# Kernel optimization log

Hardware: AMD Instinct MI355X
Metric: run time of the kernel (lower is better)

The kernel has to match this reference:

```python
import jax, jax.numpy as jnp
import numpy as np

NUM_HEADS = 16

def setup_inputs() -> dict:
    key = jax.random.key(0)
    ks = jax.random.split(key, 6)
    B, S, D = 4, 1024, 1024
    scale = 1.0 / np.sqrt(D)
    return {
        "query": jax.random.normal(ks[0], (B, S, D), jnp.float32),
        "key":   jax.random.normal(ks[1], (B, S, D), jnp.float32),
        "value": jax.random.normal(ks[2], (B, S, D), jnp.float32),
        "Wq": jax.random.normal(ks[3], (D, D), jnp.float32) * scale,
        "bq": jnp.zeros((D,), jnp.float32),
        "Wk": jax.random.normal(ks[4], (D, D), jnp.float32) * scale,
        "bk": jnp.zeros((D,), jnp.float32),
        "Wv": jax.random.normal(ks[5], (D, D), jnp.float32) * scale,
        "bv": jnp.zeros((D,), jnp.float32),
    }

def reference(query, key, value, Wq, bq, Wk, bk, Wv, bv):
    B, Sq, D = query.shape
    Sk = key.shape[1]
    H = NUM_HEADS
    dh = D // H
    # QKV projections -> (B, S, H, dh)
    q = (query @ Wq + bq).reshape(B, Sq, H, dh)
    k = (key   @ Wk + bk).reshape(B, Sk, H, dh)
    v = (value @ Wv + bv).reshape(B, Sk, H, dh)
    inv_sqrt = 1.0 / jnp.sqrt(jnp.asarray(dh, q.dtype))
    # scores: (B, H, Sq, Sk) -- attention matrix explicitly materialized (as in source)
    scores = jnp.einsum('bqhd,bkhd->bhqk', q, k) * inv_sqrt
    attn = jax.nn.softmax(scores, axis=-1)
    # context: (B, Sq, H, dh) -> (B, Sq, D)
    context = jnp.einsum('bhqk,bkhd->bqhd', attn, v).reshape(B, Sq, D)
    # source returns attn in heads-major (num_heads*batch, Sq, Sk) layout
    attn_out = jnp.transpose(attn, (1, 0, 2, 3)).reshape(H * B, Sq, Sk)
    return context, attn_out
```

## Files before the change

### kernel.cpp

```cpp
#include <hip/hip_runtime.h>

#define BB 4
#define SS 1024
#define DD 1024
#define HH 16
#define DHH 64
#define MT (BB*SS)

typedef __bf16 bf16x8 __attribute__((ext_vector_type(8)));
typedef unsigned short u16x8 __attribute__((ext_vector_type(8)));
typedef unsigned short u16x4 __attribute__((ext_vector_type(4)));
typedef float f32x4 __attribute__((ext_vector_type(4)));

__device__ __forceinline__ bf16x8 as_bf16x8(u16x8 u) {
  union { u16x8 u; bf16x8 b; } c; c.u = u; return c.b;
}
__device__ __forceinline__ unsigned short f2bf(float f) {
  unsigned int u = __float_as_uint(f);
  return (unsigned short)((u + 0x7fffu + ((u >> 16) & 1u)) >> 16);
}
__device__ __forceinline__ float bf2f(unsigned short u) {
  return __uint_as_float((unsigned int)u << 16);
}

#define MFMA(a, b, c) __builtin_amdgcn_mfma_f32_16x16x32_bf16((a), (b), (c), 0, 0, 0)

typedef const __attribute__((address_space(1))) unsigned int* gas1;
typedef __attribute__((address_space(3))) unsigned int* las3;
__device__ __forceinline__ void gl_lds16(const void* g, void* l) {
  __builtin_amdgcn_global_load_lds((gas1)g, (las3)l, 16, 0, 0);
}

__global__ __launch_bounds__(256) void conv_x3(
    const float* __restrict__ q, const float* __restrict__ k,
    const float* __restrict__ v, unsigned short* __restrict__ out)
{
  const int zz = blockIdx.y;
  const float* in = (zz == 0) ? q : (zz == 1) ? k : v;
  unsigned short* o = out + (size_t)zz * MT * DD;
  const int i = (blockIdx.x * 256 + threadIdx.x) * 8;
  float4 x0 = *(const float4*)(in + i);
  float4 x1 = *(const float4*)(in + i + 4);
  u16x8 r;
  r[0]=f2bf(x0.x); r[1]=f2bf(x0.y); r[2]=f2bf(x0.z); r[3]=f2bf(x0.w);
  r[4]=f2bf(x1.x); r[5]=f2bf(x1.y); r[6]=f2bf(x1.z); r[7]=f2bf(x1.w);
  *(u16x8*)(o + i) = r;
}

__global__ __launch_bounds__(256) void conv_wT3(
    const float* __restrict__ wq, const float* __restrict__ wk,
    const float* __restrict__ wv, unsigned short* __restrict__ out)
{
  __shared__ unsigned short Ts[64][72];
  const int zz = blockIdx.z;
  const float* W = (zz == 0) ? wq : (zz == 1) ? wk : wv;
  unsigned short* Wt = out + (size_t)zz * DD * DD;
  const int tid = threadIdx.x;
  const int n0 = blockIdx.x * 64, k0 = blockIdx.y * 64;
  const int r = tid >> 2, cs = (tid & 3) * 16;
  const float* wp = W + (size_t)(k0 + r) * DD + n0 + cs;
  #pragma unroll
  for (int c = 0; c < 4; c++) {
    float4 x = *(const float4*)(wp + c*4);
    Ts[r][cs + c*4 + 0] = f2bf(x.x); Ts[r][cs + c*4 + 1] = f2bf(x.y);
    Ts[r][cs + c*4 + 2] = f2bf(x.z); Ts[r][cs + c*4 + 3] = f2bf(x.w);
  }
  __syncthreads();
  const int nl = tid >> 2, ks = (tid & 3) * 16;
  u16x8 o0, o1;
  #pragma unroll
  for (int e = 0; e < 8; e++) { o0[e] = Ts[ks + e][nl]; o1[e] = Ts[ks + 8 + e][nl]; }
  unsigned short* op = Wt + (size_t)(n0 + nl) * DD + k0 + ks;
  *(u16x8*)op = o0;
  *(u16x8*)(op + 8) = o1;
}

__global__ __launch_bounds__(256) void gemm3(
    const unsigned short* __restrict__ X3, const unsigned short* __restrict__ Wt3,
    const float* __restrict__ bq, const float* __restrict__ bk,
    const float* __restrict__ bv, unsigned short* __restrict__ Qb,
    unsigned short* __restrict__ Kb, unsigned short* __restrict__ Vt)
{
  __shared__ union {
    struct { unsigned short A[128 * 64]; unsigned short B[64 * 64]; } s;
    unsigned short T[64][136];
  } sm;

  const int zz = blockIdx.z;
  const unsigned short* A  = X3  + (size_t)zz * MT * DD;
  const unsigned short* Bt = Wt3 + (size_t)zz * DD * DD;
  const float* bias = (zz == 0) ? bq : (zz == 1) ? bk : bv;

  const int tid  = threadIdx.x;
  const int lane = tid & 63, wave = tid >> 6;
  const int quad = lane >> 4, l16 = lane & 15;
  const int wm = (wave >> 1) * 64, wn = (wave & 1) * 32;
  const int m0 = blockIdx.x * 128, n0 = blockIdx.y * 64;
  const int lrow = lane >> 3, lcol = (lane & 7) * 8;

  f32x4 acc[4][2] = {};

  for (int k0 = 0; k0 < DD; k0 += 64) {
    #pragma unroll
    for (int r = 0; r < 4; r++) {
      const int c = wave * 4 + r;
      gl_lds16(A + (size_t)(m0 + c*8 + lrow) * DD + k0 + lcol, &sm.s.A[c * 512]);
    }
    #pragma unroll
    for (int r = 0; r < 2; r++) {
      const int c = wave * 2 + r;
      gl_lds16(Bt + (size_t)(n0 + c*8 + lrow) * DD + k0 + lcol, &sm.s.B[c * 512]);
    }
    __syncthreads();

    #pragma unroll
    for (int ks = 0; ks < 2; ks++) {
      bf16x8 af[4], bf[2];
      #pragma unroll
      for (int i = 0; i < 4; i++)
        af[i] = as_bf16x8(*(const u16x8*)&sm.s.A[(wm + i*16 + l16)*64 + ks*32 + quad*8]);
      #pragma unroll
      for (int j = 0; j < 2; j++)
        bf[j] = as_bf16x8(*(const u16x8*)&sm.s.B[(wn + j*16 + l16)*64 + ks*32 + quad*8]);
      #pragma unroll
      for (int i = 0; i < 4; i++)
        #pragma unroll
        for (int j = 0; j < 2; j++)
          acc[i][j] = MFMA(af[i], bf[j], acc[i][j]);
    }
    __syncthreads();
  }

  if (zz == 2) {
    #pragma unroll
    for (int j = 0; j < 2; j++) {
      const float bsv = bias[n0 + wn + j*16 + l16];
      #pragma unroll
      for (int i = 0; i < 4; i++)
        #pragma unroll
        for (int r = 0; r < 4; r++)
          sm.T[wn + j*16 + l16][wm + i*16 + quad*4 + r] = f2bf(acc[i][j][r] + bsv);
    }
    __syncthreads();
    const int nl = tid >> 2, mq = (tid & 3) * 32;
    unsigned short* op = Vt + (size_t)(n0 + nl) * MT + m0 + mq;
    #pragma unroll
    for (int e = 0; e < 4; e++)
      *(u16x8*)(op + e*8) = *(const u16x8*)&sm.T[nl][mq + e*8];
  } else {
    unsigned short* Out = (zz == 0) ? Qb : Kb;
    #pragma unroll
    for (int j = 0; j < 2; j++) {
      const int col = n0 + wn + j*16 + l16;
      const float bsv = bias[col];
      #pragma unroll
      for (int i = 0; i < 4; i++)
        #pragma unroll
        for (int r = 0; r < 4; r++) {
          const int row = m0 + wm + i*16 + quad*4 + r;
          Out[(size_t)row * DD + col] = f2bf(acc[i][j][r] + bsv);
        }
    }
  }
}

__global__ __launch_bounds__(256, 2) void fused_attn(
    const unsigned short* __restrict__ Qb, const unsigned short* __restrict__ Kb,
    const unsigned short* __restrict__ Vt, float* __restrict__ attn,
    float* __restrict__ ctx)
{
  __shared__ unsigned short Ps[32][1032];
  __shared__ float redm[4][32];
  __shared__ float redl[4][32];

  const int tid  = threadIdx.x;
  const int lane = tid & 63, w = tid >> 6;
  const int quad = lane >> 4, l16 = lane & 15;
  const int q0 = blockIdx.x * 32;
  const int z  = blockIdx.y;
  const int b = z & 3, h = z >> 2;
  const int cbase = w * 256;

  const unsigned short* qbase = Qb + (size_t)b * SS * DD + h * DHH;
  const unsigned short* kbase = Kb + (size_t)b * SS * DD + h * DHH;

  bf16x8 aq[2][2];
  #pragma unroll
  for (int i = 0; i < 2; i++)
    #pragma unroll
    for (int kk = 0; kk < 2; kk++)
      aq[i][kk] = as_bf16x8(*(const u16x8*)(
          qbase + (size_t)(q0 + i*16 + l16) * DD + kk*32 + quad*8));

  f32x4 acc[2][16] = {};
  #pragma unroll
  for (int t = 0; t < 16; t++) {
    const unsigned short* kp = kbase + (size_t)(cbase + t*16 + l16) * DD + quad*8;
    bf16x8 b0 = as_bf16x8(*(const u16x8*)kp);
    bf16x8 b1 = as_bf16x8(*(const u16x8*)(kp + 32));
    acc[0][t] = MFMA(aq[0][0], b0, acc[0][t]);
    acc[0][t] = MFMA(aq[0][1], b1, acc[0][t]);
    acc[1][t] = MFMA(aq[1][0], b0, acc[1][t]);
    acc[1][t] = MFMA(aq[1][1], b1, acc[1][t]);
  }

  float pm[2][4];
  #pragma unroll
  for (int i = 0; i < 2; i++)
    #pragma unroll
    for (int rr = 0; rr < 4; rr++) pm[i][rr] = -3.4e38f;
  #pragma unroll
  for (int i = 0; i < 2; i++)
    #pragma unroll
    for (int t = 0; t < 16; t++)
      #pragma unroll
      for (int rr = 0; rr < 4; rr++) pm[i][rr] = fmaxf(pm[i][rr], acc[i][t][rr]);
  #pragma unroll
  for (int off = 1; off < 16; off <<= 1)
    #pragma unroll
    for (int i = 0; i < 2; i++)
      #pragma unroll
      for (int rr = 0; rr < 4; rr++)
        pm[i][rr] = fmaxf(pm[i][rr], __shfl_xor(pm[i][rr], off));
  if (l16 == 0) {
    #pragma unroll
    for (int i = 0; i < 2; i++)
      #pragma unroll
      for (int rr = 0; rr < 4; rr++)
        redm[w][i*16 + quad*4 + rr] = pm[i][rr];
  }
  __syncthreads();
  float cc[2][4];
  #pragma unroll
  for (int i = 0; i < 2; i++)
    #pragma unroll
    for (int rr = 0; rr < 4; rr++) {
      const int r = i*16 + quad*4 + rr;
      float m = fmaxf(fmaxf(redm[0][r], redm[1][r]), fmaxf(redm[2][r], redm[3][r]));
      cc[i][rr] = m * 0.125f;
    }

  float ps[2][4] = {};
  #pragma unroll
  for (int i = 0; i < 2; i++)
    #pragma unroll
    for (int t = 0; t < 16; t++)
      #pragma unroll
      for (int rr = 0; rr < 4; rr++) {
        float e = __expf(fmaf(acc[i][t][rr], 0.125f, -cc[i][rr]));
        acc[i][t][rr] = e;
        ps[i][rr] += e;
      }
  #pragma unroll
  for (int off = 1; off < 16; off <<= 1)
    #pragma unroll
    for (int i = 0; i < 2; i++)
      #pragma unroll
      for (int rr = 0; rr < 4; rr++)
        ps[i][rr] += __shfl_xor(ps[i][rr], off);
  if (l16 == 0) {
    #pragma unroll
    for (int i = 0; i < 2; i++)
      #pragma unroll
      for (int rr = 0; rr < 4; rr++)
        redl[w][i*16 + quad*4 + rr] = ps[i][rr];
  }
  __syncthreads();
  float inv[2][4];
  #pragma unroll
  for (int i = 0; i < 2; i++)
    #pragma unroll
    for (int rr = 0; rr < 4; rr++) {
      const int r = i*16 + quad*4 + rr;
      inv[i][rr] = 1.0f / (redl[0][r] + redl[1][r] + redl[2][r] + redl[3][r]);
    }

  #pragma unroll
  for (int i = 0; i < 2; i++)
    #pragma unroll
    for (int t = 0; t < 16; t++) {
      const int col = cbase + t*16 + l16;
      #pragma unroll
      for (int rr = 0; rr < 4; rr++)
        Ps[i*16 + quad*4 + rr][col] = f2bf(acc[i][t][rr] * inv[i][rr]);
    }
  __syncthreads();

  float* slab = attn + ((size_t)z * SS + q0) * SS;
  #pragma unroll 4
  for (int j = 0; j < 32; j++) {
    const int c = j * 256 + tid;
    const int row = c >> 8, col4 = (c & 255) * 4;
    u16x4 pv = *(const u16x4*)&Ps[row][col4];
    float4 o;
    o.x = bf2f(pv[0]); o.y = bf2f(pv[1]); o.z = bf2f(pv[2]); o.w = bf2f(pv[3]);
    *(float4*)(slab + (size_t)c * 4) = o;
  }

  const unsigned short* vbase = Vt + (size_t)(h*DHH + w*16 + l16) * MT + b*SS + quad*8;
  f32x4 accp[2] = {};
  #pragma unroll 8
  for (int ks = 0; ks < 32; ks++) {
    bf16x8 bv = as_bf16x8(*(const u16x8*)(vbase + ks*32));
    bf16x8 a0 = as_bf16x8(*(const u16x8*)&Ps[l16][ks*32 + quad*8]);
    bf16x8 a1 = as_bf16x8(*(const u16x8*)&Ps[16 + l16][ks*32 + quad*8]);
    accp[0] = MFMA(a0, bv, accp[0]);
    accp[1] = MFMA(a1, bv, accp[1]);
  }
  #pragma unroll
  for (int i = 0; i < 2; i++)
    #pragma unroll
    for (int rr = 0; rr < 4; rr++)
      ctx[(size_t)(b*SS + q0 + i*16 + quad*4 + rr) * DD + h*DHH + w*16 + l16] =
          accp[i][rr];
}

extern "C" void kernel_launch(void* const* d_in, const int* in_sizes, int n_in,
                              void* d_out, int out_size, void* d_ws, size_t ws_size,
                              hipStream_t stream) {
  const float* query = (const float*)d_in[0];
  const float* key   = (const float*)d_in[1];
  const float* value = (const float*)d_in[2];
  const float* Wq    = (const float*)d_in[3];
  const float* bq    = (const float*)d_in[4];
  const float* Wk    = (const float*)d_in[5];
  const float* bk    = (const float*)d_in[6];
  const float* Wv    = (const float*)d_in[7];
  const float* bv    = (const float*)d_in[8];

  float* ctx  = (float*)d_out;
  float* attn = ctx + (size_t)BB * SS * DD;

  unsigned short* Qb = (unsigned short*)d_ws;
  unsigned short* Kb = Qb + (size_t)MT * DD;
  unsigned short* Vt = Kb + (size_t)MT * DD;

  unsigned short* X3  = (unsigned short*)attn;
  unsigned short* Wt3 = X3 + (size_t)3 * MT * DD;

  dim3 gc(MT * DD / (256 * 8), 3);
  conv_x3<<<gc, 256, 0, stream>>>(query, key, value, X3);

  dim3 gw(DD / 64, DD / 64, 3);
  conv_wT3<<<gw, 256, 0, stream>>>(Wq, Wk, Wv, Wt3);

  dim3 gg(MT / 128, DD / 64, 3);
  gemm3<<<gg, 256, 0, stream>>>(X3, Wt3, bq, bk, bv, Qb, Kb, Vt);

  dim3 g2(SS / 32, BB * HH);
  fused_attn<<<g2, 256, 0, stream>>>(Qb, Kb, Vt, attn, ctx);
}
```

Baseline: 452.5 us.

## Widen GEMM tile to 128x128, interleave attn stores with PV, add setprio

```diff
diff --git a/kernel.cpp b/kernel.cpp
--- a/kernel.cpp
+++ b/kernel.cpp
@@ -82,8 +82,8 @@
     unsigned short* __restrict__ Kb, unsigned short* __restrict__ Vt)
 {
   __shared__ union {
-    struct { unsigned short A[128 * 64]; unsigned short B[64 * 64]; } s;
-    unsigned short T[64][136];
+    struct { unsigned short A[128 * 64]; unsigned short B[128 * 64]; } s;
+    unsigned short T[128][136];
   } sm;
 
   const int zz = blockIdx.z;
@@ -94,63 +94,62 @@
   const int tid  = threadIdx.x;
   const int lane = tid & 63, wave = tid >> 6;
   const int quad = lane >> 4, l16 = lane & 15;
-  const int wm = (wave >> 1) * 64, wn = (wave & 1) * 32;
-  const int m0 = blockIdx.x * 128, n0 = blockIdx.y * 64;
+  const int wm = (wave >> 1) * 64, wn = (wave & 1) * 64;
+  const int m0 = blockIdx.x * 128, n0 = blockIdx.y * 128;
   const int lrow = lane >> 3, lcol = (lane & 7) * 8;
 
-  f32x4 acc[4][2] = {};
+  f32x4 acc[4][4] = {};
 
   for (int k0 = 0; k0 < DD; k0 += 64) {
     #pragma unroll
     for (int r = 0; r < 4; r++) {
       const int c = wave * 4 + r;
-      gl_lds16(A + (size_t)(m0 + c*8 + lrow) * DD + k0 + lcol, &sm.s.A[c * 512]);
-    }
-    #pragma unroll
-    for (int r = 0; r < 2; r++) {
-      const int c = wave * 2 + r;
+      gl_lds16(A  + (size_t)(m0 + c*8 + lrow) * DD + k0 + lcol, &sm.s.A[c * 512]);
       gl_lds16(Bt + (size_t)(n0 + c*8 + lrow) * DD + k0 + lcol, &sm.s.B[c * 512]);
     }
     __syncthreads();
 
     #pragma unroll
     for (int ks = 0; ks < 2; ks++) {
-      bf16x8 af[4], bf[2];
+      bf16x8 af[4], bfr[4];
       #pragma unroll
       for (int i = 0; i < 4; i++)
         af[i] = as_bf16x8(*(const u16x8*)&sm.s.A[(wm + i*16 + l16)*64 + ks*32 + quad*8]);
       #pragma unroll
-      for (int j = 0; j < 2; j++)
-        bf[j] = as_bf16x8(*(const u16x8*)&sm.s.B[(wn + j*16 + l16)*64 + ks*32 + quad*8]);
+      for (int j = 0; j < 4; j++)
+        bfr[j] = as_bf16x8(*(const u16x8*)&sm.s.B[(wn + j*16 + l16)*64 + ks*32 + quad*8]);
+      __builtin_amdgcn_s_setprio(1);
       #pragma unroll
       for (int i = 0; i < 4; i++)
         #pragma unroll
-        for (int j = 0; j < 2; j++)
-          acc[i][j] = MFMA(af[i], bf[j], acc[i][j]);
+        for (int j = 0; j < 4; j++)
+          acc[i][j] = MFMA(af[i], bfr[j], acc[i][j]);
+      __builtin_amdgcn_s_setprio(0);
     }
     __syncthreads();
   }
 
   if (zz == 2) {
     #pragma unroll
-    for (int j = 0; j < 2; j++) {
-      const float bsv = bias[n0 + wn + j*16 + l16];
+    for (int j = 0; j < 4; j++) {
+      const int nn = wn + j*16 + l16;
+      const float bsv = bias[n0 + nn];
       #pragma unroll
       for (int i = 0; i < 4; i++)
         #pragma unroll
         for (int r = 0; r < 4; r++)
-          sm.T[wn + j*16 + l16][wm + i*16 + quad*4 + r] = f2bf(acc[i][j][r] + bsv);
+          sm.T[nn][wm + i*16 + quad*4 + r] = f2bf(acc[i][j][r] + bsv);
     }
     __syncthreads();
-    const int nl = tid >> 2, mq = (tid & 3) * 32;
-    unsigned short* op = Vt + (size_t)(n0 + nl) * MT + m0 + mq;
-    #pragma unroll
-    for (int e = 0; e < 4; e++)
-      *(u16x8*)(op + e*8) = *(const u16x8*)&sm.T[nl][mq + e*8];
+    const int nl = tid >> 1, ms = (tid & 1) * 64;
+    unsigned short* op = Vt + (size_t)(n0 + nl) * MT + m0 + ms;
+    #pragma unroll
+    for (int e = 0; e < 8; e++)
+      *(u16x8*)(op + e*8) = *(const u16x8*)&sm.T[nl][ms + e*8];
   } else {
     unsigned short* Out = (zz == 0) ? Qb : Kb;
     #pragma unroll
-    for (int j = 0; j < 2; j++) {
+    for (int j = 0; j < 4; j++) {
       const int col = n0 + wn + j*16 + l16;
       const float bsv = bias[col];
       #pragma unroll
@@ -198,10 +197,12 @@
     const unsigned short* kp = kbase + (size_t)(cbase + t*16 + l16) * DD + quad*8;
     bf16x8 b0 = as_bf16x8(*(const u16x8*)kp);
     bf16x8 b1 = as_bf16x8(*(const u16x8*)(kp + 32));
+    __builtin_amdgcn_s_setprio(1);
     acc[0][t] = MFMA(aq[0][0], b0, acc[0][t]);
     acc[0][t] = MFMA(aq[0][1], b1, acc[0][t]);
     acc[1][t] = MFMA(aq[1][0], b0, acc[1][t]);
     acc[1][t] = MFMA(aq[1][1], b1, acc[1][t]);
+    __builtin_amdgcn_s_setprio(0);
   }
 
   float pm[2][4];
@@ -287,32 +288,29 @@
   __syncthreads();
 
   float* slab = attn + ((size_t)z * SS + q0) * SS;
-  #pragma unroll 4
-  for (int j = 0; j < 32; j++) {
-    const int c = j * 256 + tid;
-    const int row = c >> 8, col4 = (c & 255) * 4;
-    u16x4 pv = *(const u16x4*)&Ps[row][col4];
-    float4 o;
-    o.x = bf2f(pv[0]); o.y = bf2f(pv[1]); o.z = bf2f(pv[2]); o.w = bf2f(pv[3]);
-    *(float4*)(slab + (size_t)c * 4) = o;
-  }
-
   const unsigned short* vbase = Vt + (size_t)(h*DHH + w*16 + l16) * MT + b*SS + quad*8;
   f32x4 accp[2] = {};
-  #pragma unroll 8
+  #pragma unroll 4
   for (int ks = 0; ks < 32; ks++) {
     bf16x8 bv = as_bf16x8(*(const u16x8*)(vbase + ks*32));
     bf16x8 a0 = as_bf16x8(*(const u16x8*)&Ps[l16][ks*32 + quad*8]);
     bf16x8 a1 = as_bf16x8(*(const u16x8*)&Ps[16 + l16][ks*32 + quad*8]);
+    __builtin_amdgcn_s_setprio(1);
     accp[0] = MFMA(a0, bv, accp[0]);
     accp[1] = MFMA(a1, bv, accp[1]);
+    __builtin_amdgcn_s_setprio(0);
+    u16x4 pv = *(const u16x4*)&Ps[ks][tid*4];
+    f32x4 o;
+    o[0] = bf2f(pv[0]); o[1] = bf2f(pv[1]); o[2] = bf2f(pv[2]); o[3] = bf2f(pv[3]);
+    __builtin_nontemporal_store(o, (f32x4*)(slab + (size_t)ks * SS + tid*4));
   }
   #pragma unroll
   for (int i = 0; i < 2; i++)
     #pragma unroll
     for (int rr = 0; rr < 4; rr++)
-      ctx[(size_t)(b*SS + q0 + i*16 + quad*4 + rr) * DD + h*DHH + w*16 + l16] =
-          accp[i][rr];
+      __builtin_nontemporal_store(
+          accp[i][rr],
+          &ctx[(size_t)(b*SS + q0 + i*16 + quad*4 + rr) * DD + h*DHH + w*16 + l16]);
 }
 
 extern "C" void kernel_launch(void* const* d_in, const int* in_sizes, int n_in,
@@ -344,7 +342,7 @@
   dim3 gw(DD / 64, DD / 64, 3);
   conv_wT3<<<gw, 256, 0, stream>>>(Wq, Wk, Wv, Wt3);
 
-  dim3 gg(MT / 128, DD / 64, 3);
+  dim3 gg(MT / 128, DD / 128, 3);
   gemm3<<<gg, 256, 0, stream>>>(X3, Wt3, bq, bk, bv, Qb, Kb, Vt);
 
   dim3 g2(SS / 32, BB * HH);
```

Result: faster. 442.3 us (-2.2%).
